# Kernel tuning notes

Hardware: AMD Instinct MI355X
Metric: run time of the kernel (lower is better)

Reference implementation:

```python
import math
import jax, jax.numpy as jnp
import numpy as np

DIM = 1024
HEADS = 16
HEAD_DIM = DIM // HEADS
NEG = -10000.0


def setup_inputs() -> dict:
    key = jax.random.key(0)
    ks = jax.random.split(key, 9)
    B, S = 2, 2048
    s = 1.0 / math.sqrt(DIM)
    inp = {
        "x": jax.random.normal(ks[0], (B, S, DIM), dtype=jnp.float32),
        "Wq": jax.random.normal(ks[1], (DIM, DIM), dtype=jnp.float32) * s,
        "bq": jnp.zeros((DIM,), dtype=jnp.float32),
        "Wk": jax.random.normal(ks[2], (DIM, DIM), dtype=jnp.float32) * s,
        "bk": jnp.zeros((DIM,), dtype=jnp.float32),
        "Wv": jax.random.normal(ks[3], (DIM, DIM), dtype=jnp.float32) * s,
        "bv": jnp.zeros((DIM,), dtype=jnp.float32),
        "Wo": jax.random.normal(ks[4], (DIM, DIM), dtype=jnp.float32) * s,
        "bo": jnp.zeros((DIM,), dtype=jnp.float32),
    }
    return inp


def reference(x, Wq, bq, Wk, bk, Wv, bv, Wo, bo):
    B, S, D = x.shape
    q = x @ Wq + bq
    k = x @ Wk + bk
    v = x @ Wv + bv
    # [B, H, S, hd]
    def split_heads(t):
        return t.reshape(B, S, HEADS, HEAD_DIM).transpose(0, 2, 1, 3)
    q, k, v = split_heads(q), split_heads(k), split_heads(v)
    scores = jnp.einsum("bhqd,bhkd->bhqk", q, k) / math.sqrt(HEAD_DIM)
    causal = jnp.tril(jnp.ones((S, S), dtype=bool))  # [S, S]
    scores = jnp.where(causal[None, None], scores, NEG)
    probs = jax.nn.softmax(scores, axis=-1)
    ctx = jnp.einsum("bhqk,bhkd->bhqd", probs, v)  # [B, H, S, hd]
    ctx = ctx.transpose(0, 2, 1, 3).reshape(B, S, D)
    out = ctx @ Wo + bo
    return out
```

## Files before the change

### kernel.cpp

```cpp
#include <hip/hip_runtime.h>
#include <hip/hip_bf16.h>
#include <math.h>

#define DIMX 1024
#define HEADSX 16
#define HDX 64
#define BBX 2
#define SSX 2048
#define MMX (BBX*SSX)

typedef __bf16 bf16x8 __attribute__((ext_vector_type(8)));
typedef __bf16 bf16x4 __attribute__((ext_vector_type(4)));
typedef float  f32x4  __attribute__((ext_vector_type(4)));

#define NEGF (-1e30f)

static __device__ __forceinline__ void gload16(const void* g, void* l) {
  __builtin_amdgcn_global_load_lds(
      (const __attribute__((address_space(1))) unsigned int*)g,
      (__attribute__((address_space(3))) unsigned int*)l, 16, 0, 0);
}

__global__ __launch_bounds__(256) void k_convert_x(const float* __restrict__ x,
                                                   __bf16* __restrict__ xb) {
  int i = (blockIdx.x * 256 + threadIdx.x) * 4;
  float4 v = *(const float4*)&x[i];
  bf16x4 o = { (__bf16)v.x, (__bf16)v.y, (__bf16)v.z, (__bf16)v.w };
  *(bf16x4*)&xb[i] = o;
}

__global__ __launch_bounds__(256) void k_transpose_w(
    const float* __restrict__ Wq, const float* __restrict__ Wk,
    const float* __restrict__ Wv, const float* __restrict__ Wo,
    __bf16* __restrict__ wqkvT, __bf16* __restrict__ woT) {
  __shared__ __bf16 tile[64][65];
  const int mat = blockIdx.y;
  const float* src = (mat == 0) ? Wq : (mat == 1) ? Wk : (mat == 2) ? Wv : Wo;
  __bf16* dst = (mat < 3) ? (wqkvT + (size_t)mat * DIMX * DIMX) : woT;
  const int tx = blockIdx.x & 15, ty = blockIdx.x >> 4;
  const int k0 = ty * 64, n0 = tx * 64;
  #pragma unroll
  for (int rep = 0; rep < 16; ++rep) {
    int idx = rep * 256 + threadIdx.x;
    int r = idx >> 6, c = idx & 63;
    tile[r][c] = (__bf16)src[(size_t)(k0 + r) * DIMX + n0 + c];
  }
  __syncthreads();
  #pragma unroll
  for (int rep = 0; rep < 16; ++rep) {
    int idx = rep * 256 + threadIdx.x;
    int r = idx >> 6, c = idx & 63;
    dst[(size_t)(n0 + r) * DIMX + k0 + c] = tile[c][r];
  }
}

template<int EPI>
__global__ __launch_bounds__(256) void k_gemm(
    const __bf16* __restrict__ A,
    const __bf16* __restrict__ Bt,
    const float* __restrict__ b0, const float* __restrict__ b1,
    const float* __restrict__ b2,
    __bf16* __restrict__ qb, __bf16* __restrict__ kb, __bf16* __restrict__ vtb,
    float* __restrict__ outf) {
  constexpr int BK = 32, K = 1024;
  __shared__ __bf16 As[128 * BK];
  __shared__ __bf16 Bs[128 * BK];
  const int tid = threadIdx.x, lane = tid & 63, wave = tid >> 6;
  const int g = lane >> 4, r16 = lane & 15;
  const int wm = wave & 1, wn = wave >> 1;
  const int m0 = blockIdx.x * 128, n0 = blockIdx.y * 128;

  f32x4 acc[4][4] = {};

  for (int k0 = 0; k0 < K; k0 += BK) {
    __syncthreads();
    #pragma unroll
    for (int i = 0; i < 2; ++i) {
      int c = wave * 64 + lane + 256 * i;
      gload16(&A [(size_t)(m0 + (c >> 2)) * K + k0 + (c & 3) * 8],
              (char*)As + (size_t)(wave * 64 + 256 * i) * 16);
      gload16(&Bt[(size_t)(n0 + (c >> 2)) * K + k0 + (c & 3) * 8],
              (char*)Bs + (size_t)(wave * 64 + 256 * i) * 16);
    }
    __syncthreads();
    bf16x8 af[4], bfr[4];
    #pragma unroll
    for (int i = 0; i < 4; ++i)
      af[i]  = *(const bf16x8*)&As[(wm * 64 + i * 16 + r16) * BK + g * 8];
    #pragma unroll
    for (int j = 0; j < 4; ++j)
      bfr[j] = *(const bf16x8*)&Bs[(wn * 64 + j * 16 + r16) * BK + g * 8];
    #pragma unroll
    for (int i = 0; i < 4; ++i)
      #pragma unroll
      for (int j = 0; j < 4; ++j)
        acc[i][j] = __builtin_amdgcn_mfma_f32_16x16x32_bf16(af[i], bfr[j],
                                                            acc[i][j], 0, 0, 0);
  }

  #pragma unroll
  for (int i = 0; i < 4; ++i) {
    #pragma unroll
    for (int j = 0; j < 4; ++j) {
      #pragma unroll
      for (int r = 0; r < 4; ++r) {
        int m = m0 + wm * 64 + i * 16 + 4 * g + r;
        int n = n0 + wn * 64 + j * 16 + r16;
        float v = acc[i][j][r];
        if constexpr (EPI == 0) {
          int proj = n >> 10, w = n & 1023, h = w >> 6, d = w & 63;
          const float* bp = (proj == 0) ? b0 : (proj == 1) ? b1 : b2;
          v += bp[w];
          int b = m >> 11, s = m & 2047, bh = b * HEADSX + h;
          if (proj == 0)      qb [((size_t)bh * SSX + s) * HDX + d] = (__bf16)v;
          else if (proj == 1) kb [((size_t)bh * SSX + s) * HDX + d] = (__bf16)v;
          else                vtb[((size_t)bh * HDX + d) * SSX + s] = (__bf16)v;
        } else {
          outf[(size_t)m * DIMX + n] = v + b0[n];
        }
      }
    }
  }
}

__global__ __launch_bounds__(256, 2) void k_attn(
    const __bf16* __restrict__ qb, const __bf16* __restrict__ kb,
    const __bf16* __restrict__ vtb, __bf16* __restrict__ ctxb) {
  const int tid = threadIdx.x;
  const int lane = tid & 63, wq = tid >> 6;
  const int g = lane >> 4, r16 = lane & 15;

  const int id = blockIdx.x;
  const int xcd = id & 7, idx = id >> 3;
  const int bh = xcd * 4 + (idx & 3);
  const int p  = idx >> 2;
  const int b = bh >> 4, h = bh & 15;

  const int ntL = p + 1, ntH = 32 - p;
  const int q0L = p * 64 + wq * 16;
  const int q0H = (31 - p) * 64 + wq * 16;

  const __bf16* Q  = qb  + (size_t)bh * SSX * HDX;
  const __bf16* Kp = kb  + (size_t)bh * SSX * HDX;
  const __bf16* Vt = vtb + (size_t)bh * HDX * SSX;

  __shared__ __bf16 Ks[2][64 * 64];
  __shared__ __bf16 Vs[2][64 * 64];
  __shared__ unsigned Pld[4][512];

  bf16x8 qfL[2], qfH[2];
  qfL[0] = *(const bf16x8*)&Q[(size_t)(q0L + r16) * HDX + g * 8];
  qfL[1] = *(const bf16x8*)&Q[(size_t)(q0L + r16) * HDX + 32 + g * 8];
  qfH[0] = *(const bf16x8*)&Q[(size_t)(q0H + r16) * HDX + g * 8];
  qfH[1] = *(const bf16x8*)&Q[(size_t)(q0H + r16) * HDX + 32 + g * 8];

  f32x4 accL[4] = {}, accH[4] = {};
  float mrunL = NEGF, lrunL = 0.f;
  float mrunH = NEGF, lrunH = 0.f;

  const float scale2 = 0.18033688011112042f;

  auto STAGE = [&](int buf, int t) {
    const int kv0 = t * 64;
    #pragma unroll
    for (int i = 0; i < 2; ++i) {
      int c = tid + 256 * i;
      int r = c >> 3;
      int cb = (c & 7) ^ (r & 7);
      gload16(&Kp[(size_t)(kv0 + r) * HDX + cb * 8],
              (char*)Ks[buf] + (size_t)(wq * 64 + 256 * i) * 16);
      gload16(&Vt[(size_t)r * SSX + kv0 + cb * 8],
              (char*)Vs[buf] + (size_t)(wq * 64 + 256 * i) * 16);
    }
  };

  auto SUBTILE = [&](const bf16x8* qf, f32x4* acc, float& mrun, float& lrun,
                     int qrow, bool last, int kv0, int cur) {
    f32x4 sac[4] = {};
    __builtin_amdgcn_s_setprio(1);
    #pragma unroll
    for (int kk = 0; kk < 2; ++kk)
      #pragma unroll
      for (int jj = 0; jj < 4; ++jj) {
        int rr = jj * 16 + r16;
        bf16x8 kf = *(const bf16x8*)
            &Ks[cur][rr * 64 + (((kk << 2) + g) ^ (rr & 7)) * 8];
        sac[jj] = __builtin_amdgcn_mfma_f32_16x16x32_bf16(kf, qf[kk], sac[jj],
                                                          0, 0, 0);
      }
    __builtin_amdgcn_s_setprio(0);

    float pv[4][4];
    float mt = NEGF;
    #pragma unroll
    for (int jj = 0; jj < 4; ++jj)
      #pragma unroll
      for (int r = 0; r < 4; ++r) {
        float s = sac[jj][r] * scale2;
        if (last) {
          int kcol = kv0 + jj * 16 + 4 * g + r;
          s = (kcol > qrow) ? NEGF : s;
        }
        pv[jj][r] = s;
        mt = fmaxf(mt, s);
      }
    mt = fmaxf(mt, __shfl_xor(mt, 16));
    mt = fmaxf(mt, __shfl_xor(mt, 32));

    float mnew = fmaxf(mrun, mt);
    float fac = exp2f(mrun - mnew);
    mrun = mnew;

    float rs = 0.f;
    #pragma unroll
    for (int jj = 0; jj < 4; ++jj)
      #pragma unroll
      for (int r = 0; r < 4; ++r) {
        float px = exp2f(pv[jj][r] - mrun);
        pv[jj][r] = px;
        rs += px;
      }
    lrun = lrun * fac + rs;
    #pragma unroll
    for (int j2 = 0; j2 < 4; ++j2)
      #pragma unroll
      for (int r = 0; r < 4; ++r)
        acc[j2][r] *= fac;

    #pragma unroll
    for (int jj = 0; jj < 4; ++jj)
      #pragma unroll
      for (int rp = 0; rp < 2; ++rp) {
        unsigned w;
        asm("v_cvt_pk_bf16_f32 %0, %1, %2"
            : "=v"(w) : "v"(pv[jj][2 * rp]), "v"(pv[jj][2 * rp + 1]));
        int c = jj * 8 + g * 2 + rp;
        int addr = r16 * 32 + (((c >> 2) ^ (r16 & 7)) << 2) + (c & 3);
        Pld[wq][addr] = w;
      }

    bf16x8 pf[2];
    #pragma unroll
    for (int half = 0; half < 2; ++half) {
      int c = half * 16 + g * 4;
      int addr = r16 * 32 + (((c >> 2) ^ (r16 & 7)) << 2);
      pf[half] = *(const bf16x8*)&Pld[wq][addr];
    }
    __builtin_amdgcn_s_setprio(1);
    #pragma unroll
    for (int j2 = 0; j2 < 4; ++j2)
      #pragma unroll
      for (int half = 0; half < 2; ++half) {
        int dd = j2 * 16 + r16;
        bf16x8 vf = *(const bf16x8*)
            &Vs[cur][dd * 64 + (((half << 2) + g) ^ (dd & 7)) * 8];
        acc[j2] = __builtin_amdgcn_mfma_f32_16x16x32_bf16(vf, pf[half],
                                                          acc[j2], 0, 0, 0);
      }
    __builtin_amdgcn_s_setprio(0);
  };

  STAGE(0, 0);
  __syncthreads();

  for (int t = 0; t < ntH; ++t) {
    const int cur = t & 1;
    if (t + 1 < ntH) STAGE(cur ^ 1, t + 1);
    const int kv0 = t * 64;

    SUBTILE(qfH, accH, mrunH, lrunH, q0H + r16, t == ntH - 1, kv0, cur);
    if (t < ntL)
      SUBTILE(qfL, accL, mrunL, lrunL, q0L + r16, t == ntL - 1, kv0, cur);

    __syncthreads();
  }

  auto EPIL = [&](f32x4* acc, float lrun, int q0) {
    lrun += __shfl_xor(lrun, 16);
    lrun += __shfl_xor(lrun, 32);
    const float inv = 1.f / lrun;
    const int s = q0 + r16;
    #pragma unroll
    for (int j2 = 0; j2 < 4; ++j2)
      #pragma unroll
      for (int r = 0; r < 4; ++r) {
        int d = j2 * 16 + 4 * g + r;
        ctxb[((size_t)(b * SSX + s)) * DIMX + h * HDX + d] =
            (__bf16)(acc[j2][r] * inv);
      }
  };
  EPIL(accH, lrunH, q0H);
  EPIL(accL, lrunL, q0L);
}

extern "C" void kernel_launch(void* const* d_in, const int* in_sizes, int n_in,
                              void* d_out, int out_size, void* d_ws,
                              size_t ws_size, hipStream_t stream) {
  const float* x  = (const float*)d_in[0];
  const float* Wq = (const float*)d_in[1];
  const float* bq = (const float*)d_in[2];
  const float* Wk = (const float*)d_in[3];
  const float* bk = (const float*)d_in[4];
  const float* Wv = (const float*)d_in[5];
  const float* bv = (const float*)d_in[6];
  const float* Wo = (const float*)d_in[7];
  const float* bo = (const float*)d_in[8];
  float* out = (float*)d_out;

  char* ws = (char*)d_ws;
  __bf16* xb    = (__bf16*)(ws);
  __bf16* wqkvT = (__bf16*)(ws + ((size_t)8  << 20));
  __bf16* woT   = (__bf16*)(ws + ((size_t)14 << 20));
  __bf16* qb    = (__bf16*)(ws + ((size_t)16 << 20));
  __bf16* kb    = (__bf16*)(ws + ((size_t)24 << 20));
  __bf16* vtb   = (__bf16*)(ws + ((size_t)32 << 20));
  __bf16* ctxb  = xb;

  k_convert_x<<<4096, 256, 0, stream>>>(x, xb);
  k_transpose_w<<<dim3(256, 4), 256, 0, stream>>>(Wq, Wk, Wv, Wo, wqkvT, woT);
  k_gemm<0><<<dim3(32, 24), 256, 0, stream>>>(xb, wqkvT, bq, bk, bv,
                                              qb, kb, vtb, nullptr);
  k_attn<<<512, 256, 0, stream>>>(qb, kb, vtb, ctxb);
  k_gemm<1><<<dim3(32, 8), 256, 0, stream>>>(ctxb, woT, bo, nullptr, nullptr,
                                             nullptr, nullptr, nullptr, out);
}
```

Before: 121.9 us.

## Fold softmax scale into Q, skip unneeded rescales, retile out-projection GEMM

Applies the softmax scale (with the log2e factor) to Q in the QKV GEMM epilogue, which removes a multiply per score in attention. The online-softmax rescale of the accumulator and running sum now runs only when some lane's running max increases, tested with a wave-wide any. The QKV GEMM uses a 1D grid remapped so that neighbouring M tiles land on the same XCD, for better L2 reuse. The output projection gets its own 64x64-tile kernel with 1024 blocks to fill more CUs, at the cost of less reuse per block. Rounding Q to bf16 after scaling slightly changes numerics.

```diff
diff --git a/kernel.cpp b/kernel.cpp
--- a/kernel.cpp
+++ b/kernel.cpp
@@ -14,6 +14,7 @@
 typedef float  f32x4  __attribute__((ext_vector_type(4)));
 
 #define NEGF (-1e30f)
+#define QSCALE 0.18033688011112042f
 
 static __device__ __forceinline__ void gload16(const void* g, void* l) {
   __builtin_amdgcn_global_load_lds(
@@ -54,21 +55,22 @@
   }
 }
 
-template<int EPI>
-__global__ __launch_bounds__(256) void k_gemm(
+__global__ __launch_bounds__(256) void k_gemm_qkv(
     const __bf16* __restrict__ A,
     const __bf16* __restrict__ Bt,
     const float* __restrict__ b0, const float* __restrict__ b1,
     const float* __restrict__ b2,
-    __bf16* __restrict__ qb, __bf16* __restrict__ kb, __bf16* __restrict__ vtb,
-    float* __restrict__ outf) {
+    __bf16* __restrict__ qb, __bf16* __restrict__ kb, __bf16* __restrict__ vtb) {
   constexpr int BK = 32, K = 1024;
   __shared__ __bf16 As[128 * BK];
   __shared__ __bf16 Bs[128 * BK];
   const int tid = threadIdx.x, lane = tid & 63, wave = tid >> 6;
   const int g = lane >> 4, r16 = lane & 15;
   const int wm = wave & 1, wn = wave >> 1;
-  const int m0 = blockIdx.x * 128, n0 = blockIdx.y * 128;
+  const int id = blockIdx.x;
+  const int xcd = id & 7, j96 = id >> 3;
+  const int m0 = (xcd * 4 + (j96 & 3)) * 128;
+  const int n0 = (j96 >> 2) * 128;
 
   f32x4 acc[4][4] = {};
 
@@ -107,20 +109,71 @@
         int m = m0 + wm * 64 + i * 16 + 4 * g + r;
         int n = n0 + wn * 64 + j * 16 + r16;
         float v = acc[i][j][r];
-        if constexpr (EPI == 0) {
-          int proj = n >> 10, w = n & 1023, h = w >> 6, d = w & 63;
-          const float* bp = (proj == 0) ? b0 : (proj == 1) ? b1 : b2;
-          v += bp[w];
-          int b = m >> 11, s = m & 2047, bh = b * HEADSX + h;
-          if (proj == 0)      qb [((size_t)bh * SSX + s) * HDX + d] = (__bf16)v;
-          else if (proj == 1) kb [((size_t)bh * SSX + s) * HDX + d] = (__bf16)v;
-          else                vtb[((size_t)bh * HDX + d) * SSX + s] = (__bf16)v;
-        } else {
-          outf[(size_t)m * DIMX + n] = v + b0[n];
-        }
-      }
-    }
-  }
+        int proj = n >> 10, w = n & 1023, h = w >> 6, d = w & 63;
+        const float* bp = (proj == 0) ? b0 : (proj == 1) ? b1 : b2;
+        v += bp[w];
+        int b = m >> 11, s = m & 2047, bh = b * HEADSX + h;
+        if (proj == 0)      qb [((size_t)bh * SSX + s) * HDX + d] =
+                                (__bf16)(v * QSCALE);
+        else if (proj == 1) kb [((size_t)bh * SSX + s) * HDX + d] = (__bf16)v;
+        else                vtb[((size_t)bh * HDX + d) * SSX + s] = (__bf16)v;
+      }
+    }
+  }
+}
+
+__global__ __launch_bounds__(256) void k_gemm_out(
+    const __bf16* __restrict__ A,
+    const __bf16* __restrict__ Bt,
+    const float* __restrict__ bias, float* __restrict__ outf) {
+  constexpr int BK = 32, K = 1024;
+  __shared__ __bf16 As[64 * BK];
+  __shared__ __bf16 Bs[64 * BK];
+  const int tid = threadIdx.x, lane = tid & 63, wave = tid >> 6;
+  const int g = lane >> 4, r16 = lane & 15;
+  const int wm = wave & 1, wn = wave >> 1;
+  const int id = blockIdx.x;
+  const int xcd = id & 7, j128 = id >> 3;
+  const int m0 = (xcd * 8 + (j128 & 7)) * 64;
+  const int n0 = (j128 >> 3) * 64;
+
+  f32x4 acc[2][2] = {};
+
+  for (int k0 = 0; k0 < K; k0 += BK) {
+    __syncthreads();
+    {
+      int c = tid;
+      gload16(&A [(size_t)(m0 + (c >> 2)) * K + k0 + (c & 3) * 8],
+              (char*)As + (size_t)(wave * 64) * 16);
+      gload16(&Bt[(size_t)(n0 + (c >> 2)) * K + k0 + (c & 3) * 8],
+              (char*)Bs + (size_t)(wave * 64) * 16);
+    }
+    __syncthreads();
+    bf16x8 af[2], bfr[2];
+    #pragma unroll
+    for (int i = 0; i < 2; ++i)
+      af[i]  = *(const bf16x8*)&As[(wm * 32 + i * 16 + r16) * BK + g * 8];
+    #pragma unroll
+    for (int j = 0; j < 2; ++j)
+      bfr[j] = *(const bf16x8*)&Bs[(wn * 32 + j * 16 + r16) * BK + g * 8];
+    #pragma unroll
+    for (int i = 0; i < 2; ++i)
+      #pragma unroll
+      for (int j = 0; j < 2; ++j)
+        acc[i][j] = __builtin_amdgcn_mfma_f32_16x16x32_bf16(af[i], bfr[j],
+                                                            acc[i][j], 0, 0, 0);
+  }
+
+  #pragma unroll
+  for (int i = 0; i < 2; ++i)
+    #pragma unroll
+    for (int j = 0; j < 2; ++j)
+      #pragma unroll
+      for (int r = 0; r < 4; ++r) {
+        int m = m0 + wm * 32 + i * 16 + 4 * g + r;
+        int n = n0 + wn * 32 + j * 16 + r16;
+        outf[(size_t)m * DIMX + n] = acc[i][j][r] + bias[n];
+      }
 }
 
 __global__ __launch_bounds__(256, 2) void k_attn(
@@ -157,8 +210,6 @@
   f32x4 accL[4] = {}, accH[4] = {};
   float mrunL = NEGF, lrunL = 0.f;
   float mrunH = NEGF, lrunH = 0.f;
-
-  const float scale2 = 0.18033688011112042f;
 
   auto STAGE = [&](int buf, int t) {
     const int kv0 = t * 64;
@@ -196,7 +247,7 @@
     for (int jj = 0; jj < 4; ++jj)
       #pragma unroll
       for (int r = 0; r < 4; ++r) {
-        float s = sac[jj][r] * scale2;
+        float s = sac[jj][r];
         if (last) {
           int kcol = kv0 + jj * 16 + 4 * g + r;
           s = (kcol > qrow) ? NEGF : s;
@@ -207,9 +258,17 @@
     mt = fmaxf(mt, __shfl_xor(mt, 16));
     mt = fmaxf(mt, __shfl_xor(mt, 32));
 
-    float mnew = fmaxf(mrun, mt);
-    float fac = exp2f(mrun - mnew);
-    mrun = mnew;
+    if (__any(mt > mrun)) {
+      float mnew = fmaxf(mrun, mt);
+      float fac = exp2f(mrun - mnew);
+      mrun = mnew;
+      lrun *= fac;
+      #pragma unroll
+      for (int j2 = 0; j2 < 4; ++j2)
+        #pragma unroll
+        for (int r = 0; r < 4; ++r)
+          acc[j2][r] *= fac;
+    }
 
     float rs = 0.f;
     #pragma unroll
@@ -220,12 +279,7 @@
         pv[jj][r] = px;
         rs += px;
       }
-    lrun = lrun * fac + rs;
-    #pragma unroll
-    for (int j2 = 0; j2 < 4; ++j2)
-      #pragma unroll
-      for (int r = 0; r < 4; ++r)
-        acc[j2][r] *= fac;
+    lrun += rs;
 
     #pragma unroll
     for (int jj = 0; jj < 4; ++jj)
@@ -318,9 +372,7 @@
 
   k_convert_x<<<4096, 256, 0, stream>>>(x, xb);
   k_transpose_w<<<dim3(256, 4), 256, 0, stream>>>(Wq, Wk, Wv, Wo, wqkvT, woT);
-  k_gemm<0><<<dim3(32, 24), 256, 0, stream>>>(xb, wqkvT, bq, bk, bv,
-                                              qb, kb, vtb, nullptr);
+  k_gemm_qkv<<<768, 256, 0, stream>>>(xb, wqkvT, bq, bk, bv, qb, kb, vtb);
   k_attn<<<512, 256, 0, stream>>>(qb, kb, vtb, ctxb);
-  k_gemm<1><<<dim3(32, 8), 256, 0, stream>>>(ctxb, woT, bo, nullptr, nullptr,
-                                             nullptr, nullptr, nullptr, out);
-}
+  k_gemm_out<<<1024, 256, 0, stream>>>(ctxb, woT, bo, out);
+}
```

Measured after the change: 118.5 us. 1.03x faster.
